# Kernel optimization log

Hardware: AMD Instinct MI355X
Metric: run time of the kernel (lower is better)

Reference implementation:

```python
import jax, jax.numpy as jnp
import numpy as np

VOCAB, CTX, DIMS, HEAD, LAYER = 32000, 1024, 1024, 16, 4
HD = DIMS // HEAD
EPS = 1e-8


def rms_norm(x, w):
    return x * jax.lax.rsqrt(jnp.mean(x * x, axis=-1, keepdims=True) + EPS) * w


def rotary_cos_sin(ctx, inv_freq, bias):
    t = jnp.arange(ctx, dtype=jnp.float32)
    fr = t[:, None] * inv_freq[None, :] + bias[:ctx]  # [S, d/2]
    return jnp.cos(fr), jnp.sin(fr)


def apply_rotary(x, cos, sin):
    # x: [..., S, D]; cos/sin: [S, d2]; rotates first 2*d2 channels (consecutive pairs)
    d2 = cos.shape[-1]
    x1, x2 = x[..., : 2 * d2], x[..., 2 * d2 :]
    a, b = x1[..., 0::2], x1[..., 1::2]
    ra = a * cos - b * sin
    rb = a * sin + b * cos
    x1r = jnp.stack([ra, rb], axis=-1).reshape(x1.shape)
    return jnp.concatenate([x1r, x2], axis=-1)


def attention(x, lna_w, qw, qb, kw, vw, vb, ow, ob, factor, cos, sin):
    B, S, D = x.shape
    h = rms_norm(x, lna_w)
    q = h @ qw.T + qb
    k = h @ kw.T  # k has no bias
    v = h @ vw.T + vb
    split = lambda t: t.reshape(B, S, HEAD, HD).transpose(0, 2, 1, 3)  # [B,H,S,hd]
    q, k, v = split(q), split(k), split(v)
    q = apply_rotary(q, cos, sin)
    k = apply_rotary(k, cos, sin)
    scale = HD ** -0.25
    qk = jnp.einsum('bhqd,bhkd->bhqk', q * scale, k * scale)
    # scaled_mask: 0 above diagonal, 1 elsewhere (multiplicative causal mask, as in source)
    causal = jnp.tril(jnp.ones((S, S), dtype=qk.dtype))
    zero_factor = jnp.clip(jax.nn.softplus(factor), 1e-5, 0.1)
    token_ids = k[..., 0]  # [B,H,S] first key channel
    scaled_zero = jnp.where(token_ids == 0, zero_factor, jnp.ones((), qk.dtype))
    qk = qk * (causal[None, None] * scaled_zero[:, :, None, :])
    w = jax.nn.softmax(qk.astype(jnp.float32), axis=-1)
    out = jnp.einsum('bhqk,bhkd->bhqd', w, v).transpose(0, 2, 1, 3).reshape(B, S, D)
    return out @ ow.T + ob


def reference(x, xa, tok_emb, pos_emb, rot_inv_freq, rot_bias, brot_inv_freq, brot_bias,
              lna_w, q_w, q_b, k_w, v_w, v_b, o_w, o_b, factor, lnc_w,
              mlp_w1, mlp_b1, mlp_w2, mlp_b2, ln_dec_w):
    S = x.shape[1]
    h = tok_emb[x] + pos_emb[:S]  # [B,S,D]; dropout is identity in eval
    cos_d, sin_d = rotary_cos_sin(S, rot_inv_freq, rot_bias)
    h = apply_rotary(h, cos_d, sin_d)
    h = h.astype(xa.dtype)
    cos_b, sin_b = rotary_cos_sin(S, brot_inv_freq, brot_bias)
    for l in range(LAYER):
        r = h
        h = h + attention(h, lna_w[l], q_w[l], q_b[l], k_w[l], v_w[l], v_b[l],
                          o_w[l], o_b[l], factor[l], cos_b, sin_b)
        m = rms_norm(h, lnc_w[l])
        m = jax.nn.relu(m @ mlp_w1[l].T + mlp_b1[l]) @ mlp_w2[l].T + mlp_b2[l]
        h = h + m
        h = h + r  # extra residual from source
    h = rms_norm(h, ln_dec_w)
    logits = h @ tok_emb.T
    return logits


def setup_inputs() -> dict:
    key = jax.random.key(0)
    ks = jax.random.split(key, 16)
    B, S, D, L = 2, CTX, DIMS, LAYER
    tok_emb = 0.02 * jax.random.normal(ks[0], (VOCAB, D), jnp.float32)
    tok_emb = tok_emb.at[0].set(0.0)  # row 0 zeroed as in source
    inp = {
        'x': jax.random.randint(ks[1], (B, S), 0, VOCAB),
        'xa': jax.random.normal(ks[2], (B, S, D), jnp.float32),
        'tok_emb': tok_emb,
        'pos_emb': 0.02 * jax.random.normal(ks[3], (CTX, D), jnp.float32),
        'rot_inv_freq': (1.0 / 10000 ** (jnp.arange(0, D, 2, dtype=jnp.float32) / D)),
        'rot_bias': jnp.zeros((CTX, D // 2), jnp.float32),
        'brot_inv_freq': (1.0 / 10000 ** (jnp.arange(0, HD, 2, dtype=jnp.float32) / HD)),
        'brot_bias': jnp.zeros((CTX, HD // 2), jnp.float32),
        'lna_w': jnp.ones((L, D), jnp.float32),
        'q_w': 0.02 * jax.random.normal(ks[4], (L, D, D), jnp.float32),
        'q_b': jnp.zeros((L, D), jnp.float32),
        'k_w': 0.02 * jax.random.normal(ks[5], (L, D, D), jnp.float32),
        'v_w': 0.02 * jax.random.normal(ks[6], (L, D, D), jnp.float32),
        'v_b': jnp.zeros((L, D), jnp.float32),
        'o_w': 0.02 * jax.random.normal(ks[7], (L, D, D), jnp.float32),
        'o_b': jnp.zeros((L, D), jnp.float32),
        'factor': 0.001 * jnp.ones((L,), jnp.float32),
        'lnc_w': jnp.ones((L, D), jnp.float32),
        'mlp_w1': 0.02 * jax.random.normal(ks[8], (L, 4 * D, D), jnp.float32),
        'mlp_b1': jnp.zeros((L, 4 * D), jnp.float32),
        'mlp_w2': 0.02 * jax.random.normal(ks[9], (L, D, 4 * D), jnp.float32),
        'mlp_b2': jnp.zeros((L, D), jnp.float32),
        'ln_dec_w': jnp.ones((D,), jnp.float32),
    }
    return inp
```

## Files before the change

kernel.cpp:

```cpp
#include <hip/hip_runtime.h>
#include <hip/hip_bf16.h>

#define DD 1024
#define HEADS 16
#define HDIM 64
#define NLAYER 4
#define FFDIM 4096
#define NVOCAB 32000
#define SEQ 1024

typedef __bf16 bf16_t;
typedef __bf16 bf16x8 __attribute__((ext_vector_type(8)));
typedef __bf16 bf16x4 __attribute__((ext_vector_type(4)));
typedef float f32x4 __attribute__((ext_vector_type(4)));

#define MFMA16(a, b, c) __builtin_amdgcn_mfma_f32_16x16x32_bf16((a), (b), (c), 0, 0, 0)

#define GLD16(gp, lp) \
    __builtin_amdgcn_global_load_lds( \
        (const __attribute__((address_space(1))) void*)(gp), \
        (__attribute__((address_space(3))) void*)(lp), 16, 0, 0)

#define BAR() do { __builtin_amdgcn_sched_barrier(0); \
                   __builtin_amdgcn_s_barrier(); \
                   __builtin_amdgcn_sched_barrier(0); } while (0)
#define WAITVM(n) asm volatile("s_waitcnt vmcnt(" #n ")" ::: "memory")

static __device__ __forceinline__ bf16x8 pack8(float4 u, float4 v) {
    bf16x8 r;
    r[0] = (bf16_t)u.x; r[1] = (bf16_t)u.y; r[2] = (bf16_t)u.z; r[3] = (bf16_t)u.w;
    r[4] = (bf16_t)v.x; r[5] = (bf16_t)v.y; r[6] = (bf16_t)v.z; r[7] = (bf16_t)v.w;
    return r;
}

struct CvtBatch {
    const float* src[7];
    bf16_t*      dst[7];
    int          blk0[7];
    int          nseg;
};

__global__ __launch_bounds__(256) void cvt_batch(CvtBatch cb) {
    const int b = blockIdx.x;
    int s = 0;
    #pragma unroll
    for (int t = 1; t < 7; ++t)
        if (t < cb.nseg && b >= cb.blk0[t]) s = t;
    const long i = ((long)(b - cb.blk0[s]) * 256 + threadIdx.x) * 8;
    float4 a = *(const float4*)(cb.src[s] + i);
    float4 v = *(const float4*)(cb.src[s] + i + 4);
    *(bf16x8*)(cb.dst[s] + i) = pack8(a, v);
}

__global__ __launch_bounds__(256) void ropetab_kernel(
    const float* __restrict__ inv_freq, const float* __restrict__ rbias,
    float* __restrict__ ctab, float* __restrict__ stab)
{
    int idx = blockIdx.x * 256 + threadIdx.x;
    int s = idx >> 5, i = idx & 31;
    float fr = (float)s * inv_freq[i] + rbias[idx];
    ctab[idx] = cosf(fr);
    stab[idx] = sinf(fr);
}

__global__ __launch_bounds__(512) void embed_rope_kernel(
    const int* __restrict__ x, const float* __restrict__ tok_emb,
    const float* __restrict__ pos_emb, const float* __restrict__ inv_freq,
    const float* __restrict__ rbias, float* __restrict__ h, int S)
{
    const int row = blockIdx.x;
    const int s = row % S;
    const int i = threadIdx.x;
    const int tok = x[row];
    const float* e = tok_emb + (size_t)tok * DD;
    const float* p = pos_emb + (size_t)s * DD;
    float a = e[2*i]   + p[2*i];
    float b = e[2*i+1] + p[2*i+1];
    float fr = (float)s * inv_freq[i] + rbias[(size_t)s * (DD/2) + i];
    float c = cosf(fr), sn = sinf(fr);
    h[(size_t)row*DD + 2*i]   = a*c - b*sn;
    h[(size_t)row*DD + 2*i+1] = a*sn + b*c;
}

__global__ __launch_bounds__(256) void rmsnorm_kernel(
    const float* __restrict__ x, const float* __restrict__ w,
    bf16_t* __restrict__ y)
{
    const int row = blockIdx.x;
    const float* xr = x + (size_t)row * DD;
    float ss = 0.f;
    for (int j = threadIdx.x; j < DD; j += 256) { float v = xr[j]; ss += v*v; }
    for (int off = 32; off > 0; off >>= 1) ss += __shfl_down(ss, off, 64);
    __shared__ float r[4];
    if ((threadIdx.x & 63) == 0) r[threadIdx.x >> 6] = ss;
    __syncthreads();
    float tot = r[0] + r[1] + r[2] + r[3];
    float sc = rsqrtf(tot * (1.0f/(float)DD) + 1e-8f);
    for (int j = threadIdx.x; j < DD; j += 256)
        y[(size_t)row*DD + j] = (bf16_t)(xr[j] * sc * w[j]);
}

__global__ __launch_bounds__(256) void gemm_bf_s(
    const bf16_t* __restrict__ A, const bf16_t* __restrict__ W,
    const float* __restrict__ bias, const float* __restrict__ add1,
    const float* __restrict__ add2, float* __restrict__ C,
    bf16_t* __restrict__ Cb,
    int M, int N, int K, int relu, int mode)
{
    __shared__ __align__(16) bf16_t As[64*64];
    __shared__ __align__(16) bf16_t Bs[128*64];
    const int tid = threadIdx.x;
    const int m0 = blockIdx.y * 64, n0 = blockIdx.x * 128;
    const int l = tid & 63, w = tid >> 6;
    const int wr = (w >> 1) * 32, wc = (w & 1) * 64;
    const int lr = l & 15, lk = (l >> 4) * 8;

    const int srow = l >> 3, scol = (l & 7) * 8;
    const bf16_t* Ag = A + (size_t)(m0 + w*16 + srow) * K + scol;
    const bf16_t* Wg = W + (size_t)(n0 + w*32 + srow) * K + scol;

    f32x4 z4 = {0.f, 0.f, 0.f, 0.f};
    f32x4 acc[2][4];
    #pragma unroll
    for (int i = 0; i < 2; ++i)
        #pragma unroll
        for (int j = 0; j < 4; ++j) acc[i][j] = z4;

    #pragma unroll
    for (int it = 0; it < 2; ++it)
        GLD16(Ag + (size_t)(it*8)*K, As + (w*2 + it)*512);
    #pragma unroll
    for (int it = 0; it < 4; ++it)
        GLD16(Wg + (size_t)(it*8)*K, Bs + (w*4 + it)*512);

    for (int k0 = 0; k0 < K; k0 += 64) {
        __syncthreads();
        bf16x8 afr[4], bfr[8];
        #pragma unroll
        for (int kk = 0; kk < 2; ++kk) {
            #pragma unroll
            for (int i = 0; i < 2; ++i)
                afr[kk*2+i] = *(const bf16x8*)&As[(wr + i*16 + lr)*64 + kk*32 + lk];
            #pragma unroll
            for (int j = 0; j < 4; ++j)
                bfr[kk*4+j] = *(const bf16x8*)&Bs[(wc + j*16 + lr)*64 + kk*32 + lk];
        }
        __syncthreads();
        if (k0 + 64 < K) {
            #pragma unroll
            for (int it = 0; it < 2; ++it)
                GLD16(Ag + (size_t)(it*8)*K + k0 + 64, As + (w*2 + it)*512);
            #pragma unroll
            for (int it = 0; it < 4; ++it)
                GLD16(Wg + (size_t)(it*8)*K + k0 + 64, Bs + (w*4 + it)*512);
        }
        #pragma unroll
        for (int kk = 0; kk < 2; ++kk)
            #pragma unroll
            for (int i = 0; i < 2; ++i)
                #pragma unroll
                for (int j = 0; j < 4; ++j)
                    acc[i][j] = MFMA16(afr[kk*2+i], bfr[kk*4+j], acc[i][j]);
    }

    #pragma unroll
    for (int i = 0; i < 2; ++i) {
        #pragma unroll
        for (int j = 0; j < 4; ++j) {
            const int col  = n0 + wc + j*16 + lr;
            const int row0 = m0 + wr + i*16 + (l >> 4)*4;
            const float bv = bias ? bias[col] : 0.f;
            #pragma unroll
            for (int r2 = 0; r2 < 4; ++r2) {
                const int row = row0 + r2;
                float val = acc[i][j][r2] + bv;
                if (add1) val += add1[(size_t)row*N + col];
                if (add2) val += add2[(size_t)row*N + col];
                if (relu) val = fmaxf(val, 0.f);
                if (mode == 0) C[(size_t)row*N + col] = val;
                else           Cb[(size_t)row*N + col] = (bf16_t)val;
            }
        }
    }
}

__global__ __launch_bounds__(256) void gemm_bf_s64(
    const bf16_t* __restrict__ A, const bf16_t* __restrict__ W,
    const float* __restrict__ bias, const float* __restrict__ add1,
    const float* __restrict__ add2, float* __restrict__ C,
    int M, int N, int K)
{
    __shared__ __align__(16) bf16_t As[64*64];
    __shared__ __align__(16) bf16_t Bs[64*64];
    const int tid = threadIdx.x;
    const int m0 = blockIdx.y * 64, n0 = blockIdx.x * 64;
    const int l = tid & 63, w = tid >> 6;
    const int wr = (w >> 1) * 32, wc = (w & 1) * 32;
    const int lr = l & 15, lk = (l >> 4) * 8;

    const int srow = l >> 3, scol = (l & 7) * 8;
    const bf16_t* Ag = A + (size_t)(m0 + w*16 + srow) * K + scol;
    const bf16_t* Wg = W + (size_t)(n0 + w*16 + srow) * K + scol;

    f32x4 z4 = {0.f, 0.f, 0.f, 0.f};
    f32x4 acc[2][2];
    #pragma unroll
    for (int i = 0; i < 2; ++i)
        #pragma unroll
        for (int j = 0; j < 2; ++j) acc[i][j] = z4;

    #pragma unroll
    for (int it = 0; it < 2; ++it) {
        GLD16(Ag + (size_t)(it*8)*K, As + (w*2 + it)*512);
        GLD16(Wg + (size_t)(it*8)*K, Bs + (w*2 + it)*512);
    }

    for (int k0 = 0; k0 < K; k0 += 64) {
        __syncthreads();
        bf16x8 afr[4], bfr[4];
        #pragma unroll
        for (int kk = 0; kk < 2; ++kk)
            #pragma unroll
            for (int i = 0; i < 2; ++i) {
                afr[kk*2+i] = *(const bf16x8*)&As[(wr + i*16 + lr)*64 + kk*32 + lk];
                bfr[kk*2+i] = *(const bf16x8*)&Bs[(wc + i*16 + lr)*64 + kk*32 + lk];
            }
        __syncthreads();
        if (k0 + 64 < K) {
            #pragma unroll
            for (int it = 0; it < 2; ++it) {
                GLD16(Ag + (size_t)(it*8)*K + k0 + 64, As + (w*2 + it)*512);
                GLD16(Wg + (size_t)(it*8)*K + k0 + 64, Bs + (w*2 + it)*512);
            }
        }
        #pragma unroll
        for (int kk = 0; kk < 2; ++kk)
            #pragma unroll
            for (int i = 0; i < 2; ++i)
                #pragma unroll
                for (int j = 0; j < 2; ++j)
                    acc[i][j] = MFMA16(afr[kk*2+i], bfr[kk*2+j], acc[i][j]);
    }

    #pragma unroll
    for (int i = 0; i < 2; ++i) {
        #pragma unroll
        for (int j = 0; j < 2; ++j) {
            const int col  = n0 + wc + j*16 + lr;
            const int row0 = m0 + wr + i*16 + (l >> 4)*4;
            const float bv = bias ? bias[col] : 0.f;
            #pragma unroll
            for (int r2 = 0; r2 < 4; ++r2) {
                const int row = row0 + r2;
                float val = acc[i][j][r2] + bv;
                if (add1) val += add1[(size_t)row*N + col];
                if (add2) val += add2[(size_t)row*N + col];
                C[(size_t)row*N + col] = val;
            }
        }
    }
}

__global__ __launch_bounds__(512, 2) void gemm256_bf(
    const bf16_t* __restrict__ A, const bf16_t* __restrict__ W,
    float* __restrict__ C, int M, int N)
{
    extern __shared__ __align__(16) char dynsm[];
    bf16_t* TILE = (bf16_t*)dynsm;
    const int tid = threadIdx.x;
    const int nbx = gridDim.x, nby = gridDim.y;
    const int nwg = nbx * nby;
    const int lin = blockIdx.y * nbx + blockIdx.x;
    const int wg  = (lin & 7) * (nwg >> 3) + (lin >> 3);
    const int n0 = (wg / nby) * 256, m0 = (wg % nby) * 256;

    const int l = tid & 63, w = tid >> 6;
    const int wm = w >> 2, wn = w & 3;
    const int lr = l & 15, lg = l >> 4;
    const int swzr = ((l >> 1) & 7) << 3;
    const int srow = tid >> 3;
    const int scolE = ((tid & 7) * 8) ^ (((tid >> 4) & 7) << 3);

    const bf16_t* Ap = A + (size_t)m0 * 1024;
    const bf16_t* Wp = W + (size_t)n0 * 1024;

    auto STG = [&](int buf, int isB, int half, int k0) {
        const bf16_t* G = isB ? Wp : Ap;
        bf16_t* L = TILE + (buf*2 + isB)*16384 + half*8192 + w*512;
        const int rbase = half*128 + srow;
        GLD16(G + (size_t)rbase*1024 + k0 + scolE,          L);
        GLD16(G + (size_t)(rbase + 64)*1024 + k0 + scolE,   L + 4096);
    };
    auto RD_A = [&](int buf, int fi, int kk) -> bf16x8 {
        const int row = wm*128 + fi*16 + lr;
        return *(const bf16x8*)&TILE[(buf*2)*16384 + row*64 + ((kk*32 + lg*8) ^ swzr)];
    };
    auto RD_B = [&](int buf, int fj, int kk) -> bf16x8 {
        const int row = wn*64 + fj*16 + lr;
        return *(const bf16x8*)&TILE[(buf*2 + 1)*16384 + row*64 + ((kk*32 + lg*8) ^ swzr)];
    };

    f32x4 z4 = {0.f, 0.f, 0.f, 0.f};
    f32x4 acc[8][4];
    #pragma unroll
    for (int i = 0; i < 8; ++i)
        #pragma unroll
        for (int j = 0; j < 4; ++j) acc[i][j] = z4;
    bf16x8 bfr[4][2];

#define DO_PHASE(BUF, P, STAGE_STMT, TAIL_STMT) do {                          \
    bf16x8 a0_0 = RD_A(BUF, 2*(P), 0),   a0_1 = RD_A(BUF, 2*(P), 1);          \
    bf16x8 a1_0 = RD_A(BUF, 2*(P)+1, 0), a1_1 = RD_A(BUF, 2*(P)+1, 1);        \
    if ((P) == 0) {                                                           \
        _Pragma("unroll")                                                     \
        for (int fj = 0; fj < 4; ++fj) {                                      \
            bfr[fj][0] = RD_B(BUF, fj, 0);                                    \
            bfr[fj][1] = RD_B(BUF, fj, 1);                                    \
        }                                                                     \
    }                                                                         \
    STAGE_STMT;                                                               \
    BAR();                                                                    \
    __builtin_amdgcn_s_setprio(1);                                            \
    _Pragma("unroll")                                                         \
    for (int fj = 0; fj < 4; ++fj) {                                          \
        acc[2*(P)][fj]   = MFMA16(a0_0, bfr[fj][0], acc[2*(P)][fj]);          \
        acc[2*(P)][fj]   = MFMA16(a0_1, bfr[fj][1], acc[2*(P)][fj]);          \
        acc[2*(P)+1][fj] = MFMA16(a1_0, bfr[fj][0], acc[2*(P)+1][fj]);        \
        acc[2*(P)+1][fj] = MFMA16(a1_1, bfr[fj][1], acc[2*(P)+1][fj]);        \
    }                                                                         \
    __builtin_amdgcn_s_setprio(0);                                            \
    TAIL_STMT;                                                                \
    BAR();                                                                    \
} while (0)

    STG(0, 0, 0, 0);  STG(0, 0, 1, 0);
    STG(0, 1, 0, 0);  STG(0, 1, 1, 0);
    STG(1, 1, 0, 64); STG(1, 1, 1, 64);
    WAITVM(4);
    BAR();

    #pragma unroll 1
    for (int itr = 0; itr < 8; ++itr) {
        const int k_o  = (2*itr + 1) * 64;
        const int k_e2 = (2*itr + 2) * 64;
        const int k_o2 = (2*itr + 3) * 64;
        const bool more = (itr < 7);
        DO_PHASE(0, 0, STG(1, 0, 0, k_o), ;);
        DO_PHASE(0, 1, STG(1, 0, 1, k_o), ;);
        DO_PHASE(0, 2, if (more) STG(0, 1, 0, k_e2), ;);
        DO_PHASE(0, 3, if (more) STG(0, 1, 1, k_e2),
                 if (more) { WAITVM(4); } else { WAITVM(0); });
        DO_PHASE(1, 0, if (more) STG(0, 0, 0, k_e2), ;);
        DO_PHASE(1, 1, if (more) STG(0, 0, 1, k_e2), ;);
        DO_PHASE(1, 2, if (more) STG(1, 1, 0, k_o2), ;);
        DO_PHASE(1, 3, if (more) STG(1, 1, 1, k_o2),
                 if (more) { WAITVM(4); });
    }
#undef DO_PHASE

    #pragma unroll
    for (int i = 0; i < 8; ++i) {
        #pragma unroll
        for (int j = 0; j < 4; ++j) {
            const int col  = n0 + wn*64 + j*16 + lr;
            const int row0 = m0 + wm*128 + i*16 + lg*4;
            #pragma unroll
            for (int r2 = 0; r2 < 4; ++r2)
                C[(size_t)(row0 + r2)*N + col] = acc[i][j][r2];
        }
    }
}

__global__ __launch_bounds__(256) void gemm_bfw32(
    const bf16_t* __restrict__ A, const float* __restrict__ W,
    float* __restrict__ C, int M, int N, int K)
{
    __shared__ __align__(16) bf16_t As[128*64];
    __shared__ __align__(16) bf16_t Bs[128*64];
    const int tid = threadIdx.x;
    const int m0 = blockIdx.y * 128, n0 = blockIdx.x * 128;
    const int l = tid & 63, w = tid >> 6;
    const int wr = (w >> 1) * 64, wc = (w & 1) * 64;
    const int lr = l & 15, lk = (l >> 4) * 8;
    const int srow = l >> 3, scol = (l & 7) * 8;
    const bf16_t* Ag = A + (size_t)(m0 + w*32 + srow) * K + scol;
    const int r = tid >> 1, half = (tid & 1) * 32;
    const float* Wp = W + (size_t)(n0 + r) * K + half;

    f32x4 z4 = {0.f, 0.f, 0.f, 0.f};
    f32x4 acc[4][4];
    #pragma unroll
    for (int i = 0; i < 4; ++i)
        #pragma unroll
        for (int j = 0; j < 4; ++j) acc[i][j] = z4;

    for (int k0 = 0; k0 < K; k0 += 64) {
        float4 wv[8];
        #pragma unroll
        for (int j = 0; j < 8; ++j) wv[j] = *(const float4*)(Wp + k0 + 4*j);
        __syncthreads();
        #pragma unroll
        for (int it = 0; it < 4; ++it)
            GLD16(Ag + (size_t)(it*8)*K + k0, As + (w*4 + it)*512);
        #pragma unroll
        for (int j = 0; j < 4; ++j)
            *(bf16x8*)&Bs[r*64 + half + 8*j] = pack8(wv[2*j], wv[2*j+1]);
        __syncthreads();
        #pragma unroll
        for (int kk = 0; kk < 2; ++kk) {
            bf16x8 afr[4], bfr[4];
            #pragma unroll
            for (int i = 0; i < 4; ++i)
                afr[i] = *(const bf16x8*)&As[(wr + i*16 + lr)*64 + kk*32 + lk];
            #pragma unroll
            for (int j = 0; j < 4; ++j)
                bfr[j] = *(const bf16x8*)&Bs[(wc + j*16 + lr)*64 + kk*32 + lk];
            #pragma unroll
            for (int i = 0; i < 4; ++i)
                #pragma unroll
                for (int j = 0; j < 4; ++j)
                    acc[i][j] = MFMA16(afr[i], bfr[j], acc[i][j]);
        }
    }
    #pragma unroll
    for (int i = 0; i < 4; ++i)
        #pragma unroll
        for (int j = 0; j < 4; ++j) {
            const int col  = n0 + wc + j*16 + lr;
            const int row0 = m0 + wr + i*16 + (l >> 4)*4;
            #pragma unroll
            for (int r2 = 0; r2 < 4; ++r2)
                C[(size_t)(row0 + r2)*N + col] = acc[i][j][r2];
        }
}

__global__ __launch_bounds__(256) void qkv_gemm(
    const bf16_t* __restrict__ A, const bf16_t* __restrict__ Wq,
    const bf16_t* __restrict__ Wk, const bf16_t* __restrict__ Wv,
    const float* __restrict__ qb, const float* __restrict__ vbias,
    const float* __restrict__ ctab, const float* __restrict__ stab,
    const float* __restrict__ fptr,
    bf16_t* __restrict__ qbf, bf16_t* __restrict__ kbf,
    bf16_t* __restrict__ vt, int S)
{
    __shared__ __align__(16) bf16_t smem[12288];
    bf16_t* As = smem;
    bf16_t* Bs = smem + 4096;
    const int tid = threadIdx.x;
    const int seg = blockIdx.x >> 3;
    const int n0  = (blockIdx.x & 7) * 128;
    const int m0  = blockIdx.y * 64;
    const bf16_t* W = (seg == 0) ? Wq : (seg == 1) ? Wk : Wv;
    const int K = DD;
    const int l = tid & 63, w = tid >> 6;
    const int wr = (w >> 1) * 32, wc = (w & 1) * 64;
    const int lr = l & 15, lk = (l >> 4) * 8;
    const int g4 = l >> 4;

    const int srow = l >> 3, scol = (l & 7) * 8;
    const bf16_t* Ag = A + (size_t)(m0 + w*16 + srow) * K + scol;
    const bf16_t* Wg = W + (size_t)(n0 + w*32 + srow) * K + scol;

    f32x4 z4 = {0.f, 0.f, 0.f, 0.f};
    f32x4 acc[2][4];
    #pragma unroll
    for (int i = 0; i < 2; ++i)
        #pragma unroll
        for (int j = 0; j < 4; ++j) acc[i][j] = z4;

    #pragma unroll
    for (int it = 0; it < 2; ++it)
        GLD16(Ag + (size_t)(it*8)*K, As + (w*2 + it)*512);
    #pragma unroll
    for (int it = 0; it < 4; ++it)
        GLD16(Wg + (size_t)(it*8)*K, Bs + (w*4 + it)*512);

    for (int k0 = 0; k0 < K; k0 += 64) {
        __syncthreads();
        bf16x8 afr[4], bfr[8];
        #pragma unroll
        for (int kk = 0; kk < 2; ++kk) {
            #pragma unroll
            for (int i = 0; i < 2; ++i)
                afr[kk*2+i] = *(const bf16x8*)&As[(wr + i*16 + lr)*64 + kk*32 + lk];
            #pragma unroll
            for (int j = 0; j < 4; ++j)
                bfr[kk*4+j] = *(const bf16x8*)&Bs[(wc + j*16 + lr)*64 + kk*32 + lk];
        }
        __syncthreads();
        if (k0 + 64 < K) {
            #pragma unroll
            for (int it = 0; it < 2; ++it)
                GLD16(Ag + (size_t)(it*8)*K + k0 + 64, As + (w*2 + it)*512);
            #pragma unroll
            for (int it = 0; it < 4; ++it)
                GLD16(Wg + (size_t)(it*8)*K + k0 + 64, Bs + (w*4 + it)*512);
        }
        #pragma unroll
        for (int kk = 0; kk < 2; ++kk)
            #pragma unroll
            for (int i = 0; i < 2; ++i)
                #pragma unroll
                for (int j = 0; j < 4; ++j)
                    acc[i][j] = MFMA16(afr[kk*2+i], bfr[kk*4+j], acc[i][j]);
    }

    float zf = 0.f;
    if (seg == 1) {
        float f = fptr[0];
        float sp = (f > 20.f) ? f : log1pf(expf(f));
        zf = fminf(fmaxf(sp, 1e-5f), 0.1f);
    }

    #pragma unroll
    for (int i = 0; i < 2; ++i) {
        float ov[4][4];
        #pragma unroll
        for (int j = 0; j < 4; ++j) {
            const int col = n0 + wc + j*16 + lr;
            const float bv = (seg == 0) ? qb[col] : (seg == 2) ? vbias[col] : 0.f;
            const int d  = col & 63;
            const int pi = d >> 1;
            #pragma unroll
            for (int r2 = 0; r2 < 4; ++r2) {
                const int row = m0 + wr + i*16 + g4*4 + r2;
                const int s  = row & (SEQ - 1);
                float val = acc[i][j][r2] + bv;
                if (seg < 2) {
                    float partner = __shfl_xor(val, 1, 64);
                    float c  = ctab[s*32 + pi];
                    float sn = stab[s*32 + pi];
                    val = ((d & 1) == 0) ? (val*c - partner*sn)
                                         : (partner*sn + val*c);
                }
                ov[j][r2] = val;
            }
        }
        if (seg == 1) {
            #pragma unroll
            for (int r2 = 0; r2 < 4; ++r2) {
                float z0 = __shfl(ov[0][r2], (l & 48), 64);
                float zr = (z0 == 0.0f) ? zf : 1.0f;
                #pragma unroll
                for (int j = 0; j < 4; ++j) ov[j][r2] *= zr;
            }
        }
        #pragma unroll
        for (int j = 0; j < 4; ++j) {
            const int col = n0 + wc + j*16 + lr;
            #pragma unroll
            for (int r2 = 0; r2 < 4; ++r2) {
                const int row = m0 + wr + i*16 + g4*4 + r2;
                if (seg == 0)      qbf[(size_t)row*DD + col] = (bf16_t)ov[j][r2];
                else if (seg == 1) kbf[(size_t)row*DD + col] = (bf16_t)ov[j][r2];
                else smem[(col - n0)*66 + (row - m0)] = (bf16_t)ov[j][r2];
            }
        }
    }

    if (seg == 2) {
        __syncthreads();
        const int bb2 = m0 >> 10, s0 = m0 & (SEQ - 1);
        const int d2 = tid >> 1, sh = (tid & 1) * 32;
        const int hh2 = (n0 >> 6) + (d2 >> 6);
        const int dd2 = d2 & 63;
        bf16_t* dst = vt + ((size_t)(bb2*HEADS + hh2)*HDIM + dd2)*S + s0 + sh;
        const bf16_t* srcp = smem + d2*66 + sh;
        #pragma unroll
        for (int k2 = 0; k2 < 4; ++k2)
            *(bf16x8*)(dst + k2*8) = *(const bf16x8*)(srcp + k2*8);
    }
}

__global__ __launch_bounds__(256) void attn_fused(
    const bf16_t* __restrict__ qbf, const bf16_t* __restrict__ kbf,
    const bf16_t* __restrict__ Vt, bf16_t* __restrict__ O, int S)
{
    __shared__ __align__(16) bf16_t Ks[128*64];
    __shared__ __align__(16) bf16_t Vs[64*128];
    __shared__ __align__(16) bf16_t Ps[64*128];

    const int tid = threadIdx.x;
    const int qt = (gridDim.x - 1) - blockIdx.x;
    const int q0 = qt * 64;
    const int bh = blockIdx.y, b = bh >> 4, hh = bh & 15;
    const int l = tid & 63, w = tid >> 6;
    const int lr = l & 15, g = l >> 4;
    const int lk = g * 8;
    const int ktm = q0 >> 7;
    const int cnt = S - 128*(ktm + 1);
    const int myq = q0 + w*16 + lr;
    const int qloc = w*16 + lr;

    bf16x8 qfr[2];
    {
        const bf16_t* qp = qbf + (size_t)(b*S + myq)*DD + hh*HDIM;
        qfr[0] = *(const bf16x8*)(qp + lk);
        qfr[1] = *(const bf16x8*)(qp + 32 + lk);
    }

    float m_run = (cnt > 0) ? 0.f : -3.0e38f;
    float psum = 0.f;
    f32x4 z4 = {0.f, 0.f, 0.f, 0.f};
    f32x4 acc[4];
    #pragma unroll
    for (int j = 0; j < 4; ++j) acc[j] = z4;

    const int sr = l >> 3, sc = (l & 7) * 8;

    for (int kt = 0; kt <= ktm; ++kt) {
        __syncthreads();
        const bf16_t* Kg = kbf + (size_t)(b*S + kt*128)*DD + hh*HDIM;
        #pragma unroll
        for (int it = 0; it < 4; ++it) {
            const int krow = (w*4 + it)*8 + sr;
            GLD16(Kg + (size_t)krow*DD + sc, Ks + (w*4 + it)*512);
        }
        const bf16_t* Vg = Vt + ((size_t)bh*HDIM)*S + kt*128;
        #pragma unroll
        for (int it = 0; it < 4; ++it) {
            const int drow = (w*4 + it)*4 + g;
            GLD16(Vg + (size_t)drow*S + lr*8, Vs + (w*4 + it)*512);
        }
        __syncthreads();

        float sv[8][4];
        float mtile = -3.0e38f;
        #pragma unroll
        for (int f = 0; f < 8; ++f) {
            bf16x8 ka0 = *(const bf16x8*)&Ks[(f*16 + lr)*64 + lk];
            bf16x8 ka1 = *(const bf16x8*)&Ks[(f*16 + lr)*64 + 32 + lk];
            f32x4 t = z4;
            t = MFMA16(ka0, qfr[0], t);
            t = MFMA16(ka1, qfr[1], t);
            #pragma unroll
            for (int r = 0; r < 4; ++r) {
                const int key = kt*128 + f*16 + g*4 + r;
                float v = t[r] * 0.125f;
                v = (key <= myq) ? v : 0.f;
                sv[f][r] = v;
                mtile = fmaxf(mtile, v);
            }
        }
        mtile = fmaxf(mtile, __shfl_xor(mtile, 16, 64));
        mtile = fmaxf(mtile, __shfl_xor(mtile, 32, 64));
        const float m_new = fmaxf(m_run, mtile);
        const float fac = expf(m_run - m_new);
        m_run = m_new;

        float ps_t = 0.f;
        #pragma unroll
        for (int f = 0; f < 8; ++f) {
            bf16x4 pk;
            #pragma unroll
            for (int r = 0; r < 4; ++r) {
                float p = expf(sv[f][r] - m_new);
                ps_t += p;
                pk[r] = (bf16_t)p;
            }
            const int byteoff = (qloc*256 + f*32 + g*8) ^ ((lr & 7) << 4);
            *(bf16x4*)((char*)Ps + byteoff) = pk;
        }
        ps_t += __shfl_xor(ps_t, 16, 64);
        ps_t += __shfl_xor(ps_t, 32, 64);
        psum = psum * fac + ps_t;

        #pragma unroll
        for (int r = 0; r < 4; ++r) {
            const float fr_ = __shfl(fac, g*4 + r, 64);
            #pragma unroll
            for (int j = 0; j < 4; ++j) acc[j][r] *= fr_;
        }

        #pragma unroll
        for (int kk = 0; kk < 4; ++kk) {
            const int rboff = (qloc*256 + kk*64 + g*16) ^ ((lr & 7) << 4);
            bf16x8 pa = *(const bf16x8*)((char*)Ps + rboff);
            #pragma unroll
            for (int j = 0; j < 4; ++j) {
                bf16x8 vb = *(const bf16x8*)&Vs[(j*16 + lr)*128 + kk*32 + lk];
                acc[j] = MFMA16(pa, vb, acc[j]);
            }
        }
    }

    float vtail = 0.f;
    if (cnt > 0) {
        psum += (float)cnt * expf(-m_run);
        const bf16_t* vp = Vt + ((size_t)bh*HDIM + l)*S + 128*(ktm + 1);
        for (int k = 0; k < cnt; k += 8) {
            bf16x8 v = *(const bf16x8*)(vp + k);
            #pragma unroll
            for (int e = 0; e < 8; ++e) vtail += (float)v[e];
        }
    }

    #pragma unroll
    for (int r = 0; r < 4; ++r) {
        const float m_r  = __shfl(m_run, g*4 + r, 64);
        const float ps_r = __shfl(psum,  g*4 + r, 64);
        const float inv = 1.0f / ps_r;
        const float tailf = (cnt > 0) ? expf(-m_r) : 0.f;
        const int qrow = q0 + w*16 + g*4 + r;
        const size_t rowbase = (size_t)(b*S + qrow)*DD + hh*HDIM;
        #pragma unroll
        for (int j = 0; j < 4; ++j) {
            const float vt_j = __shfl(vtail, j*16 + lr, 64);
            float val = acc[j][r];
            if (cnt > 0) val += tailf * vt_j;
            O[rowbase + j*16 + lr] = (bf16_t)(val * inv);
        }
    }
}

extern "C" void kernel_launch(void* const* d_in, const int* in_sizes, int n_in,
                              void* d_out, int out_size, void* d_ws, size_t ws_size,
                              hipStream_t stream)
{
    const int S = SEQ;
    const int B = in_sizes[0] / S;
    const int M = B * S;
    const int BH = B * HEADS;

    const int*   x       = (const int*)  d_in[0];
    const float* tok_emb = (const float*)d_in[2];
    const float* pos_emb = (const float*)d_in[3];
    const float* rif     = (const float*)d_in[4];
    const float* rbias   = (const float*)d_in[5];
    const float* brif    = (const float*)d_in[6];
    const float* bbias   = (const float*)d_in[7];
    const float* lna     = (const float*)d_in[8];
    const float* qw      = (const float*)d_in[9];
    const float* qb      = (const float*)d_in[10];
    const float* kw      = (const float*)d_in[11];
    const float* vw      = (const float*)d_in[12];
    const float* vbias   = (const float*)d_in[13];
    const float* ow      = (const float*)d_in[14];
    const float* ob      = (const float*)d_in[15];
    const float* factor  = (const float*)d_in[16];
    const float* lnc     = (const float*)d_in[17];
    const float* w1      = (const float*)d_in[18];
    const float* b1      = (const float*)d_in[19];
    const float* w2      = (const float*)d_in[20];
    const float* b2      = (const float*)d_in[21];
    const float* lnd     = (const float*)d_in[22];

    char* ob_ = (char*)d_out;
    const size_t MiB = 1024*1024;
    float*  h      = (float*)(ob_ + 0*MiB);
    float*  h2     = (float*)(ob_ + 8*MiB);
    bf16_t* qbf    = (bf16_t*)(ob_ + 16*MiB);
    bf16_t* kbf    = (bf16_t*)(ob_ + 20*MiB);
    bf16_t* vt     = (bf16_t*)(ob_ + 24*MiB);
    bf16_t* attno  = (bf16_t*)(ob_ + 28*MiB);
    bf16_t* m1     = (bf16_t*)(ob_ + 32*MiB);
    float*  ctab   = (float*)(ob_ + 50*MiB);
    float*  stab   = (float*)(ob_ + 51*MiB);
    bf16_t* qw_bf  = (bf16_t*)(ob_ + 64*MiB);
    bf16_t* kw_bf  = (bf16_t*)(ob_ + 72*MiB);
    bf16_t* vw_bf  = (bf16_t*)(ob_ + 80*MiB);
    bf16_t* ow_bf  = (bf16_t*)(ob_ + 88*MiB);
    bf16_t* w1_bf  = (bf16_t*)(ob_ + 96*MiB);
    bf16_t* w2_bf  = (bf16_t*)(ob_ + 128*MiB);

    bf16_t* hn      = (bf16_t*)d_ws;
    bf16_t* temb_bf = (bf16_t*)((char*)d_ws + 4*MiB);
    const bool big_ws = ws_size >= (size_t)(70*MiB);

    {
        CvtBatch cb;
        const float* srcs[7] = {qw, kw, vw, ow, w1, w2, tok_emb};
        bf16_t*      dsts[7] = {qw_bf, kw_bf, vw_bf, ow_bf, w1_bf, w2_bf, temb_bf};
        const long   ns[7]   = {(long)NLAYER*DD*DD, (long)NLAYER*DD*DD,
                                (long)NLAYER*DD*DD, (long)NLAYER*DD*DD,
                                (long)NLAYER*FFDIM*DD, (long)NLAYER*FFDIM*DD,
                                (long)NVOCAB*DD};
        int nseg = big_ws ? 7 : 6;
        int acc = 0;
        for (int s = 0; s < 7; ++s) {
            cb.src[s] = srcs[s]; cb.dst[s] = dsts[s];
            cb.blk0[s] = acc;
            if (s < nseg) acc += (int)(ns[s] / 2048);
        }
        cb.nseg = nseg;
        cvt_batch<<<acc, 256, 0, stream>>>(cb);
    }
    ropetab_kernel<<<(S*32)/256, 256, 0, stream>>>(brif, bbias, ctab, stab);

    dim3 gMLP1(FFDIM/128, M/64);
    dim3 gS64(DD/64,    M/64);
    dim3 gV256(NVOCAB/256, M/256);
    dim3 gVfb(NVOCAB/128, M/128);
    dim3 gQKV(3*8, M/64);
    dim3 gATT(S/64, BH);

    embed_rope_kernel<<<M, 512, 0, stream>>>(x, tok_emb, pos_emb, rif, rbias, h, S);

    for (int l = 0; l < NLAYER; ++l) {
        const size_t wo = (size_t)l * DD * DD;
        const size_t fo = (size_t)l * FFDIM * DD;
        rmsnorm_kernel<<<M, 256, 0, stream>>>(h, lna + l*DD, hn);
        qkv_gemm<<<gQKV, 256, 0, stream>>>(hn, qw_bf + wo, kw_bf + wo, vw_bf + wo,
                                           qb + l*DD, vbias + l*DD, ctab, stab,
                                           factor + l, qbf, kbf, vt, S);
        attn_fused<<<gATT, 256, 0, stream>>>(qbf, kbf, vt, attno, S);
        gemm_bf_s64<<<gS64, 256, 0, stream>>>(attno, ow_bf + wo, ob + l*DD, h, nullptr,
                                              h2, M, DD, DD);
        rmsnorm_kernel<<<M, 256, 0, stream>>>(h2, lnc + l*DD, hn);
        gemm_bf_s<<<gMLP1, 256, 0, stream>>>(hn, w1_bf + fo, b1 + l*FFDIM, nullptr,
                                             nullptr, nullptr, m1, M, FFDIM, DD, 1, 1);
        gemm_bf_s64<<<gS64, 256, 0, stream>>>(m1, w2_bf + fo, b2 + l*DD, h2, h,
                                              h, M, DD, FFDIM);
    }

    rmsnorm_kernel<<<M, 256, 0, stream>>>(h, lnd, hn);
    if (big_ws) {
        hipFuncSetAttribute((const void*)gemm256_bf,
                            hipFuncAttributeMaxDynamicSharedMemorySize, 131072);
        gemm256_bf<<<gV256, 512, 131072, stream>>>(hn, temb_bf, (float*)d_out,
                                                   M, NVOCAB);
    } else {
        gemm_bfw32<<<gVfb, 256, 0, stream>>>(hn, tok_emb, (float*)d_out, M, NVOCAB, DD);
    }
}
```

Baseline: 1.066 ms.

## XOR-swizzle LDS tiles in GEMMs and attention; widen weight conversion per thread

Applies an XOR swizzle to the column offset used when global_load_lds writes 16-byte chunks into shared memory. The same swizzle is applied to the fragment reads in the GEMM kernels and to the K/V tiles in attention, to reduce LDS bank conflicts on the MFMA operand loads. Separately, the fp32-to-bf16 weight conversion kernel now handles 16 elements per thread with half as many blocks, cutting launch and indexing overhead. The swizzle must match exactly between the writers and every reader, or results will be wrong.

```diff
diff --git a/kernel.cpp b/kernel.cpp
--- a/kernel.cpp
+++ b/kernel.cpp
@@ -46,10 +46,13 @@
     #pragma unroll
     for (int t = 1; t < 7; ++t)
         if (t < cb.nseg && b >= cb.blk0[t]) s = t;
-    const long i = ((long)(b - cb.blk0[s]) * 256 + threadIdx.x) * 8;
-    float4 a = *(const float4*)(cb.src[s] + i);
-    float4 v = *(const float4*)(cb.src[s] + i + 4);
-    *(bf16x8*)(cb.dst[s] + i) = pack8(a, v);
+    const long i = ((long)(b - cb.blk0[s]) * 256 + threadIdx.x) * 16;
+    float4 a0 = *(const float4*)(cb.src[s] + i);
+    float4 a1 = *(const float4*)(cb.src[s] + i + 4);
+    float4 a2 = *(const float4*)(cb.src[s] + i + 8);
+    float4 a3 = *(const float4*)(cb.src[s] + i + 12);
+    *(bf16x8*)(cb.dst[s] + i)     = pack8(a0, a1);
+    *(bf16x8*)(cb.dst[s] + i + 8) = pack8(a2, a3);
 }
 
 __global__ __launch_bounds__(256) void ropetab_kernel(
@@ -114,10 +117,12 @@
     const int l = tid & 63, w = tid >> 6;
     const int wr = (w >> 1) * 32, wc = (w & 1) * 64;
     const int lr = l & 15, lk = (l >> 4) * 8;
-
-    const int srow = l >> 3, scol = (l & 7) * 8;
-    const bf16_t* Ag = A + (size_t)(m0 + w*16 + srow) * K + scol;
-    const bf16_t* Wg = W + (size_t)(n0 + w*32 + srow) * K + scol;
+    const int swz = (lr & 7) << 3;
+
+    const int srow = l >> 3;
+    const int scolS = 8 * ((l & 7) ^ (l >> 3));
+    const bf16_t* Ag = A + (size_t)(m0 + w*16 + srow) * K + scolS;
+    const bf16_t* Wg = W + (size_t)(n0 + w*32 + srow) * K + scolS;
 
     f32x4 z4 = {0.f, 0.f, 0.f, 0.f};
     f32x4 acc[2][4];
@@ -140,10 +145,10 @@
         for (int kk = 0; kk < 2; ++kk) {
             #pragma unroll
             for (int i = 0; i < 2; ++i)
-                afr[kk*2+i] = *(const bf16x8*)&As[(wr + i*16 + lr)*64 + kk*32 + lk];
+                afr[kk*2+i] = *(const bf16x8*)&As[(wr + i*16 + lr)*64 + ((kk*32 + lk) ^ swz)];
             #pragma unroll
             for (int j = 0; j < 4; ++j)
-                bfr[kk*4+j] = *(const bf16x8*)&Bs[(wc + j*16 + lr)*64 + kk*32 + lk];
+                bfr[kk*4+j] = *(const bf16x8*)&Bs[(wc + j*16 + lr)*64 + ((kk*32 + lk) ^ swz)];
         }
         __syncthreads();
         if (k0 + 64 < K) {
@@ -197,10 +202,12 @@
     const int l = tid & 63, w = tid >> 6;
     const int wr = (w >> 1) * 32, wc = (w & 1) * 32;
     const int lr = l & 15, lk = (l >> 4) * 8;
-
-    const int srow = l >> 3, scol = (l & 7) * 8;
-    const bf16_t* Ag = A + (size_t)(m0 + w*16 + srow) * K + scol;
-    const bf16_t* Wg = W + (size_t)(n0 + w*16 + srow) * K + scol;
+    const int swz = (lr & 7) << 3;
+
+    const int srow = l >> 3;
+    const int scolS = 8 * ((l & 7) ^ (l >> 3));
+    const bf16_t* Ag = A + (size_t)(m0 + w*16 + srow) * K + scolS;
+    const bf16_t* Wg = W + (size_t)(n0 + w*16 + srow) * K + scolS;
 
     f32x4 z4 = {0.f, 0.f, 0.f, 0.f};
     f32x4 acc[2][2];
@@ -222,8 +229,8 @@
         for (int kk = 0; kk < 2; ++kk)
             #pragma unroll
             for (int i = 0; i < 2; ++i) {
-                afr[kk*2+i] = *(const bf16x8*)&As[(wr + i*16 + lr)*64 + kk*32 + lk];
-                bfr[kk*2+i] = *(const bf16x8*)&Bs[(wc + i*16 + lr)*64 + kk*32 + lk];
+                afr[kk*2+i] = *(const bf16x8*)&As[(wr + i*16 + lr)*64 + ((kk*32 + lk) ^ swz)];
+                bfr[kk*2+i] = *(const bf16x8*)&Bs[(wc + i*16 + lr)*64 + ((kk*32 + lk) ^ swz)];
             }
         __syncthreads();
         if (k0 + 64 < K) {
@@ -456,10 +463,12 @@
     const int wr = (w >> 1) * 32, wc = (w & 1) * 64;
     const int lr = l & 15, lk = (l >> 4) * 8;
     const int g4 = l >> 4;
-
-    const int srow = l >> 3, scol = (l & 7) * 8;
-    const bf16_t* Ag = A + (size_t)(m0 + w*16 + srow) * K + scol;
-    const bf16_t* Wg = W + (size_t)(n0 + w*32 + srow) * K + scol;
+    const int swz = (lr & 7) << 3;
+
+    const int srow = l >> 3;
+    const int scolS = 8 * ((l & 7) ^ (l >> 3));
+    const bf16_t* Ag = A + (size_t)(m0 + w*16 + srow) * K + scolS;
+    const bf16_t* Wg = W + (size_t)(n0 + w*32 + srow) * K + scolS;
 
     f32x4 z4 = {0.f, 0.f, 0.f, 0.f};
     f32x4 acc[2][4];
@@ -482,10 +491,10 @@
         for (int kk = 0; kk < 2; ++kk) {
             #pragma unroll
             for (int i = 0; i < 2; ++i)
-                afr[kk*2+i] = *(const bf16x8*)&As[(wr + i*16 + lr)*64 + kk*32 + lk];
+                afr[kk*2+i] = *(const bf16x8*)&As[(wr + i*16 + lr)*64 + ((kk*32 + lk) ^ swz)];
             #pragma unroll
             for (int j = 0; j < 4; ++j)
-                bfr[kk*4+j] = *(const bf16x8*)&Bs[(wc + j*16 + lr)*64 + kk*32 + lk];
+                bfr[kk*4+j] = *(const bf16x8*)&Bs[(wc + j*16 + lr)*64 + ((kk*32 + lk) ^ swz)];
         }
         __syncthreads();
         if (k0 + 64 < K) {
@@ -587,6 +596,7 @@
     const int l = tid & 63, w = tid >> 6;
     const int lr = l & 15, g = l >> 4;
     const int lk = g * 8;
+    const int swz = (lr & 7) << 3;
     const int ktm = q0 >> 7;
     const int cnt = S - 128*(ktm + 1);
     const int myq = q0 + w*16 + lr;
@@ -606,7 +616,10 @@
     #pragma unroll
     for (int j = 0; j < 4; ++j) acc[j] = z4;
 
-    const int sr = l >> 3, sc = (l & 7) * 8;
+    const int sr = l >> 3;
+    const int scK = 8 * ((l & 7) ^ (l >> 3));
+    const int scV0 = (lr * 8) ^ ((4*0 + g) << 3);
+    const int scV1 = (lr * 8) ^ ((4*1 + g) << 3);
 
     for (int kt = 0; kt <= ktm; ++kt) {
         __syncthreads();
@@ -614,13 +627,14 @@
         #pragma unroll
         for (int it = 0; it < 4; ++it) {
             const int krow = (w*4 + it)*8 + sr;
-            GLD16(Kg + (size_t)krow*DD + sc, Ks + (w*4 + it)*512);
+            GLD16(Kg + (size_t)krow*DD + scK, Ks + (w*4 + it)*512);
         }
         const bf16_t* Vg = Vt + ((size_t)bh*HDIM)*S + kt*128;
         #pragma unroll
         for (int it = 0; it < 4; ++it) {
             const int drow = (w*4 + it)*4 + g;
-            GLD16(Vg + (size_t)drow*S + lr*8, Vs + (w*4 + it)*512);
+            GLD16(Vg + (size_t)drow*S + ((it & 1) ? scV1 : scV0),
+                  Vs + (w*4 + it)*512);
         }
         __syncthreads();
 
@@ -628,8 +642,8 @@
         float mtile = -3.0e38f;
         #pragma unroll
         for (int f = 0; f < 8; ++f) {
-            bf16x8 ka0 = *(const bf16x8*)&Ks[(f*16 + lr)*64 + lk];
-            bf16x8 ka1 = *(const bf16x8*)&Ks[(f*16 + lr)*64 + 32 + lk];
+            bf16x8 ka0 = *(const bf16x8*)&Ks[(f*16 + lr)*64 + (lk ^ swz)];
+            bf16x8 ka1 = *(const bf16x8*)&Ks[(f*16 + lr)*64 + ((32 + lk) ^ swz)];
             f32x4 t = z4;
             t = MFMA16(ka0, qfr[0], t);
             t = MFMA16(ka1, qfr[1], t);
@@ -678,7 +692,7 @@
             bf16x8 pa = *(const bf16x8*)((char*)Ps + rboff);
             #pragma unroll
             for (int j = 0; j < 4; ++j) {
-                bf16x8 vb = *(const bf16x8*)&Vs[(j*16 + lr)*128 + kk*32 + lk];
+                bf16x8 vb = *(const bf16x8*)&Vs[(j*16 + lr)*128 + ((kk*32 + lk) ^ swz)];
                 acc[j] = MFMA16(pa, vb, acc[j]);
             }
         }
@@ -780,7 +794,7 @@
         for (int s = 0; s < 7; ++s) {
             cb.src[s] = srcs[s]; cb.dst[s] = dsts[s];
             cb.blk0[s] = acc;
-            if (s < nseg) acc += (int)(ns[s] / 2048);
+            if (s < nseg) acc += (int)(ns[s] / 4096);
         }
         cb.nseg = nseg;
         cvt_batch<<<acc, 256, 0, stream>>>(cb);
```

Result: faster. 944.0 us (-11.4%).
